# Kernel tuning notes

Measured on AMD Instinct MI355X. Metric: run time of the kernel, lower is better.

## Reference

```python
import jax, jax.numpy as jnp
import numpy as np

VOCAB = 21128; EMBED = 768; D_MODEL = 256; H = 100; NTAGS = 21; B = 32; T = 256


def setup_inputs() -> dict:
    key = jax.random.key(0)
    ks = jax.random.split(key, 18)
    n = lambda k, s, sc=0.05: jax.random.normal(k, s, dtype=jnp.float32) * sc
    return {
        "words": jax.random.randint(ks[0], (B, T), 0, VOCAB),
        "target": jax.random.randint(ks[1], (B, T), 0, NTAGS),
        "embed_table": n(ks[2], (VOCAB, EMBED), 1.0),
        "in_fc_w": n(ks[3], (D_MODEL, EMBED)),
        "in_fc_b": n(ks[4], (D_MODEL,)),
        "Wih0": n(ks[5], (2, 4 * H, D_MODEL)),
        "Whh0": n(ks[6], (2, 4 * H, H)),
        "bih0": n(ks[7], (2, 4 * H)),
        "bhh0": n(ks[8], (2, 4 * H)),
        "Wih1": n(ks[9], (2, 4 * H, 2 * H)),
        "Whh1": n(ks[10], (2, 4 * H, H)),
        "bih1": n(ks[11], (2, 4 * H)),
        "bhh1": n(ks[12], (2, 4 * H)),
        "out_w": n(ks[13], (NTAGS, 2 * H)),
        "out_b": n(ks[14], (NTAGS,)),
        "trans": n(ks[15], (NTAGS, NTAGS)),
        "start_s": n(ks[16], (NTAGS,)),
        "end_s": n(ks[17], (NTAGS,)),
    }


def _lstm_dir(x, Wih, Whh, bih, bhh, reverse):
    # x: (T, B, D); torch LSTM gate order i, f, g, o
    Bsz, Hd = x.shape[1], Whh.shape[1]
    pre = jnp.einsum('tbd,gd->tbg', x, Wih) + bih  # precompute input projection

    def step(carry, p):
        h, c = carry
        g = p + h @ Whh.T + bhh
        i, f, gg, o = jnp.split(g, 4, axis=-1)
        c = jax.nn.sigmoid(f) * c + jax.nn.sigmoid(i) * jnp.tanh(gg)
        h = jax.nn.sigmoid(o) * jnp.tanh(c)
        return (h, c), h

    init = (jnp.zeros((Bsz, Hd), x.dtype), jnp.zeros((Bsz, Hd), x.dtype))
    _, hs = jax.lax.scan(step, init, pre, reverse=reverse)
    return hs


def _bilstm(x, layers):
    h = x
    for (Wih, Whh, bih, bhh) in layers:  # fixed small loop over num_layers
        f = _lstm_dir(h, Wih[0], Whh[0], bih[0], bhh[0], False)
        b = _lstm_dir(h, Wih[1], Whh[1], bih[1], bhh[1], True)
        h = jnp.concatenate([f, b], axis=-1)
    return h


def _crf_loss(logits, tags, mask, trans, start_s, end_s):
    # fastNLP ConditionalRandomField loss: normalizer - gold_score, per batch elem
    lt = jnp.swapaxes(logits, 0, 1)          # (T, B, N)
    tt = tags.T                               # (T, B)
    mt = mask.T.astype(logits.dtype)          # (T, B)
    alpha0 = lt[0] + start_s

    def step(alpha, inp):
        emit, m = inp
        tmp = alpha[:, :, None] + trans[None] + emit[:, None, :]  # (B, N, N)
        new = jax.nn.logsumexp(tmp, axis=1)
        return jnp.where(m[:, None] > 0, new, alpha), None

    alpha, _ = jax.lax.scan(step, alpha0, (lt[1:], mt[1:]))
    normalizer = jax.nn.logsumexp(alpha + end_s, axis=1)  # (B,)

    emit_sc = jnp.take_along_axis(lt, tt[..., None], axis=2)[..., 0] * mt
    trans_sc = trans[tt[:-1], tt[1:]] * mt[1:]
    seq_lens = mask.sum(axis=1)
    last_idx = jnp.maximum(seq_lens - 1, 0)
    last_tags = tags[jnp.arange(tags.shape[0]), last_idx]
    gold = emit_sc.sum(0) + trans_sc.sum(0) + start_s[tt[0]] + end_s[last_tags]
    return normalizer - gold


def reference(words, target, embed_table, in_fc_w, in_fc_b, Wih0, Whh0, bih0, bhh0,
              Wih1, Whh1, bih1, bhh1, out_w, out_b, trans, start_s, end_s):
    mask = words != 0
    x = embed_table[words]                       # (B, T, E)
    x = x @ in_fc_w.T + in_fc_b                  # (B, T, D)
    x = jnp.swapaxes(x, 0, 1)                    # (T, B, D)
    h = _bilstm(x, [(Wih0, Whh0, bih0, bhh0), (Wih1, Whh1, bih1, bhh1)])
    h = jnp.swapaxes(h, 0, 1)                    # (B, T, 2H); dropout is identity at eval
    logits = jax.nn.log_softmax(h @ out_w.T + out_b, axis=-1)
    return _crf_loss(logits, target, mask, trans, start_s, end_s)  # (B,)
```

## Files before the change

### kernel.cpp

```cpp
#include <hip/hip_runtime.h>
#include <hip/hip_bf16.h>

#define VOCAB 21128
#define EMBED 768
#define DMODEL 256
#define HID 100
#define NTAGS 21
#define BB 32
#define TT 256
#define NTOK (BB*TT)

typedef float f32x4 __attribute__((ext_vector_type(4)));
typedef unsigned int u32x4 __attribute__((ext_vector_type(4)));
typedef short s16x8 __attribute__((ext_vector_type(8)));

__device__ __forceinline__ float sigm(float x) { return 1.0f / (1.0f + __expf(-x)); }
__device__ __forceinline__ float tanh_(float x) { return 2.0f / (1.0f + __expf(-2.0f * x)) - 1.0f; }

__device__ __forceinline__ unsigned int bfr(float x) {
    unsigned int u = __float_as_uint(x);
    return (u + 0x7fffu + ((u >> 16) & 1u)) >> 16;
}
__device__ __forceinline__ unsigned int bfpack(float lo, float hi) {
    return (bfr(hi) << 16) | bfr(lo);
}
__device__ __forceinline__ unsigned int cvtpk(float lo, float hi) {
    unsigned int r;
    asm("v_cvt_pk_bf16_f32 %0, %1, %2" : "=v"(r) : "v"(lo), "v"(hi));
    return r;
}
__device__ __forceinline__ s16x8 asfrag(u32x4 v) {
    union { u32x4 u; s16x8 s; } x; x.u = v; return x.s;
}

#define BAR() do { \
    asm volatile("s_waitcnt lgkmcnt(0)" ::: "memory"); \
    __builtin_amdgcn_s_barrier(); \
    __builtin_amdgcn_sched_barrier(0); \
} while (0)

__global__ __launch_bounds__(256) void gemm_mfma(
    const float* __restrict__ A, int lda,
    const float* __restrict__ B, int ldb,
    const float* __restrict__ bias1, const float* __restrict__ bias2,
    float* __restrict__ C, int ldc,
    int N, int K,
    const int* __restrict__ gatherWords, int permGates)
{
    __shared__ unsigned int As_[2][4096];
    __shared__ unsigned int Bs_[2][2048];

    const int tid = threadIdx.x;
    const int row0 = blockIdx.x * 128;
    const int col0 = blockIdx.y * 64;
    const int lane = tid & 63;
    const int wave = tid >> 6;
    const int wr = wave >> 1, wc = wave & 1;
    const int nsteps = (K + 63) >> 6;

    const float* arow[8]; int aoff[8]; int kqA[8];
    #pragma unroll
    for (int j = 0; j < 8; ++j) {
        int v = tid + 256 * j;
        int row = v >> 4, kq = v & 15;
        int grow = row0 + row;
        const float* ap;
        if (gatherWords) {
            int widx = gatherWords[(grow & 31) * TT + (grow >> 5)];
            ap = A + (size_t)widx * lda;
        } else {
            ap = A + (size_t)grow * lda;
        }
        arow[j] = ap + 4 * kq;
        aoff[j] = (row >> 4) * 512 + (kq >> 3) * 256 + ((kq >> 1) & 3) * 64
                + (row & 15) * 4 + (kq & 1) * 2;
        kqA[j] = kq;
    }
    const float* brow[4]; int boff[4]; int bok[4]; int kqB[4];
    #pragma unroll
    for (int j = 0; j < 4; ++j) {
        int v = tid + 256 * j;
        int r = v >> 4, kq = v & 15;
        int gcol = col0 + r;
        bok[j] = (gcol < N);
        int src = bok[j] ? gcol : 0;
        if (permGates && bok[j]) {
            int d2 = (gcol >= 400) ? 1 : 0;
            int rr = gcol - d2 * 400;
            src = d2 * 400 + (rr & 3) * 100 + (rr >> 2);
        }
        brow[j] = B + (size_t)src * ldb + 4 * kq;
        boff[j] = (r >> 4) * 512 + (kq >> 3) * 256 + ((kq >> 1) & 3) * 64
                + (r & 15) * 4 + (kq & 1) * 2;
        kqB[j] = kq;
    }

    {
        #pragma unroll
        for (int j = 0; j < 8; ++j) {
            f32x4 v = {0.f,0.f,0.f,0.f};
            if (4 * kqA[j] < K) v = *(const f32x4*)(arow[j]);
            As_[0][aoff[j]]     = cvtpk(v.x, v.y);
            As_[0][aoff[j] + 1] = cvtpk(v.z, v.w);
        }
        #pragma unroll
        for (int j = 0; j < 4; ++j) {
            f32x4 v = {0.f,0.f,0.f,0.f};
            if (bok[j] && 4 * kqB[j] < K) v = *(const f32x4*)(brow[j]);
            Bs_[0][boff[j]]     = cvtpk(v.x, v.y);
            Bs_[0][boff[j] + 1] = cvtpk(v.z, v.w);
        }
    }
    BAR();

    f32x4 acc[4][2] = {};

    for (int s = 0; s < nsteps; ++s) {
        const int cur = s & 1, nxt = cur ^ 1;

        f32x4 la[8], lb[4];
        if (s + 1 < nsteps) {
            const int kb = (s + 1) * 64;
            #pragma unroll
            for (int j = 0; j < 8; ++j) {
                la[j] = (f32x4){0.f,0.f,0.f,0.f};
                if (kb + 4 * kqA[j] < K) la[j] = *(const f32x4*)(arow[j] + kb);
            }
            #pragma unroll
            for (int j = 0; j < 4; ++j) {
                lb[j] = (f32x4){0.f,0.f,0.f,0.f};
                if (bok[j] && kb + 4 * kqB[j] < K) lb[j] = *(const f32x4*)(brow[j] + kb);
            }
        }

        u32x4 af[2][4], bf2[2][2];
        #pragma unroll
        for (int f = 0; f < 2; ++f) {
            #pragma unroll
            for (int mt = 0; mt < 4; ++mt)
                af[f][mt] = *(const u32x4*)&As_[cur][(4 * wr + mt) * 512 + f * 256 + lane * 4];
            #pragma unroll
            for (int nt = 0; nt < 2; ++nt)
                bf2[f][nt] = *(const u32x4*)&Bs_[cur][(2 * wc + nt) * 512 + f * 256 + lane * 4];
        }
        #pragma unroll
        for (int f = 0; f < 2; ++f)
            #pragma unroll
            for (int mt = 0; mt < 4; ++mt)
                #pragma unroll
                for (int nt = 0; nt < 2; ++nt)
                    acc[mt][nt] = __builtin_amdgcn_mfma_f32_16x16x32_bf16(
                        asfrag(af[f][mt]), asfrag(bf2[f][nt]), acc[mt][nt], 0, 0, 0);

        if (s + 1 < nsteps) {
            #pragma unroll
            for (int j = 0; j < 8; ++j) {
                As_[nxt][aoff[j]]     = cvtpk(la[j].x, la[j].y);
                As_[nxt][aoff[j] + 1] = cvtpk(la[j].z, la[j].w);
            }
            #pragma unroll
            for (int j = 0; j < 4; ++j) {
                Bs_[nxt][boff[j]]     = cvtpk(lb[j].x, lb[j].y);
                Bs_[nxt][boff[j] + 1] = cvtpk(lb[j].z, lb[j].w);
            }
        }
        BAR();
    }

    const int r4 = (lane >> 4) * 4;
    const int cl = lane & 15;
    #pragma unroll
    for (int nt = 0; nt < 2; ++nt) {
        int gcol = col0 + (2 * wc + nt) * 16 + cl;
        if (gcol < N) {
            int src = gcol;
            if (permGates) {
                int d2 = (gcol >= 400) ? 1 : 0;
                int rr = gcol - d2 * 400;
                src = d2 * 400 + (rr & 3) * 100 + (rr >> 2);
            }
            float bv = bias1[src];
            if (bias2) bv += bias2[src];
            #pragma unroll
            for (int mt = 0; mt < 4; ++mt) {
                int grow = row0 + (4 * wr + mt) * 16 + r4;
                #pragma unroll
                for (int r = 0; r < 4; ++r)
                    C[(size_t)(grow + r) * ldc + gcol] = acc[mt][nt][r] + bv;
            }
        }
    }
}

#define STASH_FRAG(SS, F, A0,A1,A2,A3) { \
    int tile = base + (SS); if (tile > 24) tile = 24; \
    int row16 = 16*tile + m16; \
    const float* srcp = Whh + (size_t)(dir*400 + (row16 & 3)*100 + (row16 >> 2)) * HID; \
    const int k0 = 32*(F) + 8*g4; \
    f32x4 fa = {0.f,0.f,0.f,0.f}, fb = {0.f,0.f,0.f,0.f}; \
    if (k0 < HID) fa = *(const f32x4*)(srcp + k0); \
    if (k0 + 4 < HID) fb = *(const f32x4*)(srcp + k0 + 4); \
    unsigned p0 = bfpack(fa.x, fa.y), p1 = bfpack(fa.z, fa.w); \
    unsigned p2 = bfpack(fb.x, fb.y), p3 = bfpack(fb.z, fb.w); \
    asm volatile("v_accvgpr_write_b32 a" #A0 ", %0\n\t" \
                 "v_accvgpr_write_b32 a" #A1 ", %1\n\t" \
                 "v_accvgpr_write_b32 a" #A2 ", %2\n\t" \
                 "v_accvgpr_write_b32 a" #A3 ", %3" \
                 :: "v"(p0), "v"(p1), "v"(p2), "v"(p3) \
                 : "a" #A0, "a" #A1, "a" #A2, "a" #A3); }

#define MF(ACC, BF, A0, A3) \
    asm volatile("v_mfma_f32_16x16x32_bf16 %0, a[" #A0 ":" #A3 "], %1, %0" \
                 : "+v"(ACC) : "v"(BF));

#define LOADCHUNK(K2) { \
    const int s0_ = 16 * (K2); \
    _Pragma("unroll") \
    for (int j = 0; j < 7; ++j) { \
        if (okj[j]) { \
            int tg = dir ? (TT - 1 - (s0_ + sicj[j])) : (s0_ + sicj[j]); \
            rr[j] = *(const f32x4*)(pre + (size_t)(tg * BB + b) * 800 + dir * 400 + 4 * gqj[j]); \
        } \
    } }

#define WRITECHUNK(BUF) { \
    _Pragma("unroll") \
    for (int j = 0; j < 7; ++j) { \
        if (okj[j]) { \
            float* p_ = &preS[(BUF) * 6400 + sicj[j] * 400 + gqj[j]]; \
            p_[0]   = rr[j].x; \
            p_[100] = rr[j].y; \
            p_[200] = rr[j].z; \
            p_[300] = rr[j].w; \
        } \
    } }

#define LSTM_STEP(SIC) { \
    const int t_ = dir ? (TT - 1 - (s0 + (SIC))) : (s0 + (SIC)); \
    const int i_ = t_ * BB + b; \
    const u32x4* hb_ = (const u32x4*)&h16[(SIC) & 1][0]; \
    u32x4 bf0 = hb_[g4], bf1 = hb_[4+g4], bf2 = hb_[8+g4], bf3 = hb_[12+g4]; \
    const float* pp_ = &preS[curbase + (SIC) * 400 + my_u]; \
    float px = pp_[0], py = pp_[100], pz = pp_[200], pw = pp_[300]; \
    f32x4 acc0 = {0.f,0.f,0.f,0.f}, acc1 = {0.f,0.f,0.f,0.f}; \
    f32x4 acc2 = {0.f,0.f,0.f,0.f}, acc3 = {0.f,0.f,0.f,0.f}; \
    f32x4 acc4 = {0.f,0.f,0.f,0.f}, acc5 = {0.f,0.f,0.f,0.f}; \
    f32x4 acc6 = {0.f,0.f,0.f,0.f}; \
    asm volatile("s_nop 1"); \
    MF(acc0, bf0, 0, 3)    MF(acc1, bf0, 16, 19)  MF(acc2, bf0, 32, 35) \
    MF(acc3, bf0, 48, 51)  MF(acc4, bf0, 64, 67)  MF(acc5, bf0, 80, 83) \
    MF(acc6, bf0, 96, 99) \
    MF(acc0, bf1, 4, 7)    MF(acc1, bf1, 20, 23)  MF(acc2, bf1, 36, 39) \
    MF(acc3, bf1, 52, 55)  MF(acc4, bf1, 68, 71)  MF(acc5, bf1, 84, 87) \
    MF(acc6, bf1, 100, 103) \
    MF(acc0, bf2, 8, 11)   MF(acc1, bf2, 24, 27)  MF(acc2, bf2, 40, 43) \
    MF(acc3, bf2, 56, 59)  MF(acc4, bf2, 72, 75)  MF(acc5, bf2, 88, 91) \
    MF(acc6, bf2, 104, 107) \
    MF(acc0, bf3, 12, 15)  MF(acc1, bf3, 28, 31)  MF(acc2, bf3, 44, 47) \
    MF(acc3, bf3, 60, 63)  MF(acc4, bf3, 76, 79)  MF(acc5, bf3, 92, 95) \
    MF(acc6, bf3, 108, 111) \
    asm volatile("s_nop 7\n\ts_nop 7"); \
    f32x4 t01 = (slot_sel & 1) ? acc1 : acc0; \
    f32x4 t23 = (slot_sel & 1) ? acc3 : acc2; \
    f32x4 t45 = (slot_sel & 1) ? acc5 : acc4; \
    f32x4 u0 = (slot_sel & 2) ? t23 : t01; \
    f32x4 u1 = (slot_sel & 2) ? acc6 : t45; \
    f32x4 sel = (slot_sel & 4) ? u1 : u0; \
    float igt = sigm(sel.x + px); \
    float fgt = sigm(sel.y + py); \
    float ggt = tanh_(sel.z + pz); \
    float ogt = sigm(sel.w + pw); \
    c = fgt * c + igt * ggt; \
    float h = ogt * tanh_(c); \
    if (writer) { \
        h16[((SIC) + 1) & 1][my_u] = (unsigned short)bfr(h); \
        hout[(size_t)i_ * 200 + dir * HID + my_u] = h; \
    } \
    BAR(); }

__global__ __launch_bounds__(256, 1) void lstm_mfma(
    const float* __restrict__ pre,
    const float* __restrict__ Whh,
    float* __restrict__ hout)
{
    const int dir = blockIdx.x >> 5;
    const int b = blockIdx.x & 31;
    const int tid = threadIdx.x;
    const int wave = tid >> 6;
    const int lane = tid & 63;
    const int m16 = lane & 15;
    const int g4 = lane >> 4;
    const int slot_sel = lane & 7;

    const int base = (wave == 0) ? 0 : (wave == 1) ? 7 : (wave == 2) ? 13 : 19;

    __shared__ alignas(16) unsigned short h16[2][128];
    __shared__ alignas(16) float preS[2 * 6400];

    STASH_FRAG(0,0, 0,1,2,3)      STASH_FRAG(0,1, 4,5,6,7)
    STASH_FRAG(0,2, 8,9,10,11)    STASH_FRAG(0,3, 12,13,14,15)
    STASH_FRAG(1,0, 16,17,18,19)  STASH_FRAG(1,1, 20,21,22,23)
    STASH_FRAG(1,2, 24,25,26,27)  STASH_FRAG(1,3, 28,29,30,31)
    STASH_FRAG(2,0, 32,33,34,35)  STASH_FRAG(2,1, 36,37,38,39)
    STASH_FRAG(2,2, 40,41,42,43)  STASH_FRAG(2,3, 44,45,46,47)
    STASH_FRAG(3,0, 48,49,50,51)  STASH_FRAG(3,1, 52,53,54,55)
    STASH_FRAG(3,2, 56,57,58,59)  STASH_FRAG(3,3, 60,61,62,63)
    STASH_FRAG(4,0, 64,65,66,67)  STASH_FRAG(4,1, 68,69,70,71)
    STASH_FRAG(4,2, 72,73,74,75)  STASH_FRAG(4,3, 76,77,78,79)
    STASH_FRAG(5,0, 80,81,82,83)  STASH_FRAG(5,1, 84,85,86,87)
    STASH_FRAG(5,2, 88,89,90,91)  STASH_FRAG(5,3, 92,93,94,95)
    STASH_FRAG(6,0, 96,97,98,99)  STASH_FRAG(6,1, 100,101,102,103)
    STASH_FRAG(6,2, 104,105,106,107) STASH_FRAG(6,3, 108,109,110,111)

    if (tid < 128) { h16[0][tid] = 0; h16[1][tid] = 0; }

    int my_tile = base + ((slot_sel < 7) ? slot_sel : 6);
    if (my_tile > 24) my_tile = 24;
    const int my_u = 4 * my_tile + g4;
    const int ow_lim = (wave == 0) ? 7 : 6;
    const bool writer = (slot_sel < ow_lim) && ((lane & 8) == 0);

    int sicj[7], gqj[7]; bool okj[7];
    #pragma unroll
    for (int j = 0; j < 7; ++j) {
        int idx = tid + 256 * j;
        okj[j] = (idx < 1600);
        int ic = okj[j] ? idx : 0;
        sicj[j] = ic / 100;
        gqj[j] = ic - 100 * sicj[j];
    }

    float c = 0.f;
    f32x4 rr[7];

    LOADCHUNK(0)
    WRITECHUNK(0)
    LOADCHUNK(1)
    BAR();

    for (int k = 0; k < 16; ++k) {
        const int s0 = 16 * k;
        const int curbase = (k & 1) * 6400;
        LSTM_STEP(0)  LSTM_STEP(1)  LSTM_STEP(2)  LSTM_STEP(3)
        LSTM_STEP(4)  LSTM_STEP(5)  LSTM_STEP(6)  LSTM_STEP(7)
        LSTM_STEP(8)  LSTM_STEP(9)  LSTM_STEP(10) LSTM_STEP(11)
        LSTM_STEP(12) LSTM_STEP(13) LSTM_STEP(14) LSTM_STEP(15)
        if (k < 15) { WRITECHUNK((k & 1) ^ 1) }
        if (k < 14) { LOADCHUNK(k + 2) }
        BAR();
    }
}

__global__ __launch_bounds__(256) void logits_lsm(
    const float* __restrict__ h1,
    const float* __restrict__ out_w,
    const float* __restrict__ out_b,
    float* __restrict__ logits)
{
    const int lane = threadIdx.x & 63;
    const int wid = (blockIdx.x * 256 + threadIdx.x) >> 6;
    const int half = lane >> 5;
    const int n = lane & 31;
    const int i = wid * 2 + half;
    if (i >= NTOK) return;

    float acc = -1e30f;
    if (n < NTAGS) {
        acc = out_b[n];
        const float4* hr = (const float4*)(h1 + (size_t)i * 200);
        const float4* wr = (const float4*)(out_w + (size_t)n * 200);
        #pragma unroll
        for (int e = 0; e < 50; ++e) {
            float4 h4 = hr[e], w4 = wr[e];
            acc += h4.x * w4.x + h4.y * w4.y + h4.z * w4.z + h4.w * w4.w;
        }
    }
    float m = acc;
    for (int off = 16; off > 0; off >>= 1) m = fmaxf(m, __shfl_xor(m, off, 32));
    float ex = (n < NTAGS) ? __expf(acc - m) : 0.f;
    float s = ex;
    for (int off = 16; off > 0; off >>= 1) s += __shfl_xor(s, off, 32);
    if (n < NTAGS) logits[(size_t)i * NTAGS + n] = acc - m - __logf(s);
}

__global__ __launch_bounds__(64) void crf_kernel(
    const float* __restrict__ logits,
    const int* __restrict__ words,
    const int* __restrict__ target,
    const float* __restrict__ trans,
    const float* __restrict__ start_s,
    const float* __restrict__ end_s,
    float* __restrict__ out)
{
    const int b = blockIdx.x;
    const int j = threadIdx.x;
    const int j21 = (j < NTAGS) ? j : (NTAGS - 1);

    float tcol[NTAGS];
    #pragma unroll
    for (int i = 0; i < NTAGS; ++i) tcol[i] = (j < NTAGS) ? trans[i * NTAGS + j] : 0.f;

    const int w0 = words[b * TT +   0 + j];
    const int w1 = words[b * TT +  64 + j];
    const int w2 = words[b * TT + 128 + j];
    const int w3 = words[b * TT + 192 + j];

    float alpha = (j < NTAGS) ? (logits[(size_t)(0 * BB + b) * NTAGS + j] + start_s[j]) : -1e30f;
    float e_cur = logits[(size_t)(1 * BB + b) * NTAGS + j21];

#define CRF_CHUNK(WREG, T0) \
    for (int u = ((T0) == 0 ? 1 : 0); u < 64; ++u) { \
        const int t = (T0) + u; \
        float e_nxt = 0.f; \
        if (t + 1 < TT) e_nxt = logits[(size_t)((t + 1) * BB + b) * NTAGS + j21]; \
        if (__shfl(WREG, u, 64) != 0) { \
            float v[NTAGS]; \
            _Pragma("unroll") \
            for (int i2 = 0; i2 < NTAGS; ++i2) \
                v[i2] = __shfl(alpha, i2, 64) + tcol[i2]; \
            float m0[11]; \
            _Pragma("unroll") \
            for (int p = 0; p < 10; ++p) m0[p] = fmaxf(v[2*p], v[2*p+1]); \
            m0[10] = v[20]; \
            float m1[6]; \
            _Pragma("unroll") \
            for (int p = 0; p < 5; ++p) m1[p] = fmaxf(m0[2*p], m0[2*p+1]); \
            m1[5] = m0[10]; \
            float m2a = fmaxf(m1[0], m1[1]), m2b = fmaxf(m1[2], m1[3]), m2c = fmaxf(m1[4], m1[5]); \
            float mx = fmaxf(fmaxf(m2a, m2b), m2c); \
            float e[NTAGS]; \
            _Pragma("unroll") \
            for (int i2 = 0; i2 < NTAGS; ++i2) e[i2] = __expf(v[i2] - mx); \
            float s0[11]; \
            _Pragma("unroll") \
            for (int p = 0; p < 10; ++p) s0[p] = e[2*p] + e[2*p+1]; \
            s0[10] = e[20]; \
            float s1[6]; \
            _Pragma("unroll") \
            for (int p = 0; p < 5; ++p) s1[p] = s0[2*p] + s0[2*p+1]; \
            s1[5] = s0[10]; \
            float ss = ((s1[0] + s1[1]) + (s1[2] + s1[3])) + (s1[4] + s1[5]); \
            float na = mx + __logf(ss) + e_cur; \
            alpha = (j < NTAGS) ? na : -1e30f; \
        } \
        e_cur = e_nxt; \
    }

    CRF_CHUNK(w0, 0)
    CRF_CHUNK(w1, 64)
    CRF_CHUNK(w2, 128)
    CRF_CHUNK(w3, 192)
#undef CRF_CHUNK

    float val = (j < NTAGS) ? (alpha + end_s[j]) : -1e30f;
    float mx = val;
    for (int off = 32; off > 0; off >>= 1) mx = fmaxf(mx, __shfl_xor(mx, off, 64));
    float s = (j < NTAGS) ? __expf(val - mx) : 0.f;
    for (int off = 32; off > 0; off >>= 1) s += __shfl_xor(s, off, 64);
    float norm = mx + __logf(s);

    float gold = 0.f, slen = 0.f;
    for (int t = j; t < TT; t += 64) {
        int tg = target[b * TT + t];
        bool m = (words[b * TT + t] != 0);
        if (m) {
            gold += logits[(size_t)(t * BB + b) * NTAGS + tg];
            slen += 1.f;
            if (t >= 1) gold += trans[target[b * TT + t - 1] * NTAGS + tg];
        }
    }
    for (int off = 32; off > 0; off >>= 1) {
        gold += __shfl_xor(gold, off, 64);
        slen += __shfl_xor(slen, off, 64);
    }
    if (j == 0) {
        int len = (int)slen;
        int last = (len > 0) ? (len - 1) : 0;
        int last_tag = target[b * TT + last];
        gold += start_s[target[b * TT + 0]] + end_s[last_tag];
        out[b] = norm - gold;
    }
}

extern "C" void kernel_launch(void* const* d_in, const int* in_sizes, int n_in,
                              void* d_out, int out_size, void* d_ws, size_t ws_size,
                              hipStream_t stream) {
    const int*   words   = (const int*)  d_in[0];
    const int*   target  = (const int*)  d_in[1];
    const float* embed   = (const float*)d_in[2];
    const float* in_fc_w = (const float*)d_in[3];
    const float* in_fc_b = (const float*)d_in[4];
    const float* Wih0    = (const float*)d_in[5];
    const float* Whh0    = (const float*)d_in[6];
    const float* bih0    = (const float*)d_in[7];
    const float* bhh0    = (const float*)d_in[8];
    const float* Wih1    = (const float*)d_in[9];
    const float* Whh1    = (const float*)d_in[10];
    const float* bih1    = (const float*)d_in[11];
    const float* bhh1    = (const float*)d_in[12];
    const float* out_w   = (const float*)d_in[13];
    const float* out_b   = (const float*)d_in[14];
    const float* trans   = (const float*)d_in[15];
    const float* start_s = (const float*)d_in[16];
    const float* end_s   = (const float*)d_in[17];
    float* out = (float*)d_out;

    float* ws = (float*)d_ws;
    float* x      = ws;
    float* pre    = ws + 2097152;
    float* h0     = ws + 8650752;
    float* h1     = ws;
    float* logits = ws + 1638400;

    gemm_mfma<<<dim3(64, 4), 256, 0, stream>>>(
        embed, EMBED, in_fc_w, EMBED, in_fc_b, nullptr,
        x, DMODEL, DMODEL, EMBED, words, 0);

    gemm_mfma<<<dim3(64, 13), 256, 0, stream>>>(
        x, DMODEL, Wih0, DMODEL, bih0, bhh0,
        pre, 800, 800, DMODEL, nullptr, 1);

    lstm_mfma<<<64, 256, 0, stream>>>(pre, Whh0, h0);

    gemm_mfma<<<dim3(64, 13), 256, 0, stream>>>(
        h0, 200, Wih1, 200, bih1, bhh1,
        pre, 800, 800, 200, nullptr, 1);

    lstm_mfma<<<64, 256, 0, stream>>>(pre, Whh1, h1);

    logits_lsm<<<NTOK / 8, 256, 0, stream>>>(h1, out_w, out_b, logits);

    crf_kernel<<<BB, 64, 0, stream>>>(logits, words, target, trans, start_s, end_s, out);
}
```

Baseline: 570.8 us.

## Batch 16 sequences per LSTM block using full MFMA N dimension

Restructures the recurrent LSTM kernel so each block handles 16 batch elements at once, putting them in the MFMA N dimension instead of running one sequence per block with the B operand mostly idle. The grid shrinks from 64 to 4 blocks. Every lane now runs the epilogue for all 7 accumulator tiles, and the LDS staging of precomputed gates is replaced by direct per-lane register prefetch two steps ahead. The trade is far fewer active CUs and more per-step epilogue work per lane, in exchange for no longer wasting MFMA throughput and no longer needing the LDS staging pass.

Result: slower. 1.339 ms (+134.6%).

```diff
diff --git a/kernel.cpp b/kernel.cpp
--- a/kernel.cpp
+++ b/kernel.cpp
@@ -193,7 +193,7 @@
 }
 
 #define STASH_FRAG(SS, F, A0,A1,A2,A3) { \
-    int tile = base + (SS); if (tile > 24) tile = 24; \
+    int tile = base + (SS); \
     int row16 = 16*tile + m16; \
     const float* srcp = Whh + (size_t)(dir*400 + (row16 & 3)*100 + (row16 >> 2)) * HID; \
     const int k0 = 32*(F) + 8*g4; \
@@ -213,68 +213,49 @@
     asm volatile("v_mfma_f32_16x16x32_bf16 %0, a[" #A0 ":" #A3 "], %1, %0" \
                  : "+v"(ACC) : "v"(BF));
 
-#define LOADCHUNK(K2) { \
-    const int s0_ = 16 * (K2); \
-    _Pragma("unroll") \
-    for (int j = 0; j < 7; ++j) { \
-        if (okj[j]) { \
-            int tg = dir ? (TT - 1 - (s0_ + sicj[j])) : (s0_ + sicj[j]); \
-            rr[j] = *(const f32x4*)(pre + (size_t)(tg * BB + b) * 800 + dir * 400 + 4 * gqj[j]); \
-        } \
-    } }
-
-#define WRITECHUNK(BUF) { \
-    _Pragma("unroll") \
-    for (int j = 0; j < 7; ++j) { \
-        if (okj[j]) { \
-            float* p_ = &preS[(BUF) * 6400 + sicj[j] * 400 + gqj[j]]; \
-            p_[0]   = rr[j].x; \
-            p_[100] = rr[j].y; \
-            p_[200] = rr[j].z; \
-            p_[300] = rr[j].w; \
-        } \
-    } }
-
-#define LSTM_STEP(SIC) { \
-    const int t_ = dir ? (TT - 1 - (s0 + (SIC))) : (s0 + (SIC)); \
-    const int i_ = t_ * BB + b; \
-    const u32x4* hb_ = (const u32x4*)&h16[(SIC) & 1][0]; \
-    u32x4 bf0 = hb_[g4], bf1 = hb_[4+g4], bf2 = hb_[8+g4], bf3 = hb_[12+g4]; \
-    const float* pp_ = &preS[curbase + (SIC) * 400 + my_u]; \
-    float px = pp_[0], py = pp_[100], pz = pp_[200], pw = pp_[300]; \
-    f32x4 acc0 = {0.f,0.f,0.f,0.f}, acc1 = {0.f,0.f,0.f,0.f}; \
-    f32x4 acc2 = {0.f,0.f,0.f,0.f}, acc3 = {0.f,0.f,0.f,0.f}; \
-    f32x4 acc4 = {0.f,0.f,0.f,0.f}, acc5 = {0.f,0.f,0.f,0.f}; \
-    f32x4 acc6 = {0.f,0.f,0.f,0.f}; \
+#define EPI(PP, SL) { \
+    f32x4 gg = ac##SL + PP##SL; \
+    float ii = sigm(gg.x); \
+    float ff = sigm(gg.y); \
+    float zz = tanh_(gg.z); \
+    float oo = sigm(gg.w); \
+    c##SL = ff * c##SL + ii * zz; \
+    float hh = oo * tanh_(c##SL); \
+    h16[nb_][bloc][u_base + 4*(SL)] = (unsigned short)bfr(hh); \
+    hout[(size_t)(t_ * BB + bb) * 200 + dir * HID + u_base + 4*(SL)] = hh; \
+}
+
+#define LSTEP(PP, S) { \
+    const int t_ = dir ? (TT - 1 - (S)) : (S); \
+    const int nb_ = ((S) + 1) & 1; \
+    const u32x4* hb_ = (const u32x4*)&h16[(S) & 1][bloc][0]; \
+    u32x4 bf0 = hb_[g4], bf1 = hb_[4 + g4], bf2 = hb_[8 + g4], bf3 = hb_[12 + g4]; \
+    f32x4 ac0 = {0.f,0.f,0.f,0.f}, ac1 = {0.f,0.f,0.f,0.f}; \
+    f32x4 ac2 = {0.f,0.f,0.f,0.f}, ac3 = {0.f,0.f,0.f,0.f}; \
+    f32x4 ac4 = {0.f,0.f,0.f,0.f}, ac5 = {0.f,0.f,0.f,0.f}; \
+    f32x4 ac6 = {0.f,0.f,0.f,0.f}; \
     asm volatile("s_nop 1"); \
-    MF(acc0, bf0, 0, 3)    MF(acc1, bf0, 16, 19)  MF(acc2, bf0, 32, 35) \
-    MF(acc3, bf0, 48, 51)  MF(acc4, bf0, 64, 67)  MF(acc5, bf0, 80, 83) \
-    MF(acc6, bf0, 96, 99) \
-    MF(acc0, bf1, 4, 7)    MF(acc1, bf1, 20, 23)  MF(acc2, bf1, 36, 39) \
-    MF(acc3, bf1, 52, 55)  MF(acc4, bf1, 68, 71)  MF(acc5, bf1, 84, 87) \
-    MF(acc6, bf1, 100, 103) \
-    MF(acc0, bf2, 8, 11)   MF(acc1, bf2, 24, 27)  MF(acc2, bf2, 40, 43) \
-    MF(acc3, bf2, 56, 59)  MF(acc4, bf2, 72, 75)  MF(acc5, bf2, 88, 91) \
-    MF(acc6, bf2, 104, 107) \
-    MF(acc0, bf3, 12, 15)  MF(acc1, bf3, 28, 31)  MF(acc2, bf3, 44, 47) \
-    MF(acc3, bf3, 60, 63)  MF(acc4, bf3, 76, 79)  MF(acc5, bf3, 92, 95) \
-    MF(acc6, bf3, 108, 111) \
+    MF(ac0, bf0, 0, 3)    MF(ac1, bf0, 16, 19)  MF(ac2, bf0, 32, 35) \
+    MF(ac3, bf0, 48, 51)  MF(ac4, bf0, 64, 67)  MF(ac5, bf0, 80, 83) \
+    MF(ac6, bf0, 96, 99) \
+    MF(ac0, bf1, 4, 7)    MF(ac1, bf1, 20, 23)  MF(ac2, bf1, 36, 39) \
+    MF(ac3, bf1, 52, 55)  MF(ac4, bf1, 68, 71)  MF(ac5, bf1, 84, 87) \
+    MF(ac6, bf1, 100, 103) \
+    MF(ac0, bf2, 8, 11)   MF(ac1, bf2, 24, 27)  MF(ac2, bf2, 40, 43) \
+    MF(ac3, bf2, 56, 59)  MF(ac4, bf2, 72, 75)  MF(ac5, bf2, 88, 91) \
+    MF(ac6, bf2, 104, 107) \
+    MF(ac0, bf3, 12, 15)  MF(ac1, bf3, 28, 31)  MF(ac2, bf3, 44, 47) \
+    MF(ac3, bf3, 60, 63)  MF(ac4, bf3, 76, 79)  MF(ac5, bf3, 92, 95) \
+    MF(ac6, bf3, 108, 111) \
     asm volatile("s_nop 7\n\ts_nop 7"); \
-    f32x4 t01 = (slot_sel & 1) ? acc1 : acc0; \
-    f32x4 t23 = (slot_sel & 1) ? acc3 : acc2; \
-    f32x4 t45 = (slot_sel & 1) ? acc5 : acc4; \
-    f32x4 u0 = (slot_sel & 2) ? t23 : t01; \
-    f32x4 u1 = (slot_sel & 2) ? acc6 : t45; \
-    f32x4 sel = (slot_sel & 4) ? u1 : u0; \
-    float igt = sigm(sel.x + px); \
-    float fgt = sigm(sel.y + py); \
-    float ggt = tanh_(sel.z + pz); \
-    float ogt = sigm(sel.w + pw); \
-    c = fgt * c + igt * ggt; \
-    float h = ogt * tanh_(c); \
-    if (writer) { \
-        h16[((SIC) + 1) & 1][my_u] = (unsigned short)bfr(h); \
-        hout[(size_t)i_ * 200 + dir * HID + my_u] = h; \
+    EPI(PP, 0) EPI(PP, 1) EPI(PP, 2) EPI(PP, 3) EPI(PP, 4) EPI(PP, 5) EPI(PP, 6) \
+    if ((S) + 2 < TT) { \
+        const int tn_ = dir ? (TT - 3 - (S)) : ((S) + 2); \
+        const float* pq_ = pre_lane + (size_t)tn_ * 25600; \
+        PP##0 = *(const f32x4*)(pq_);      PP##1 = *(const f32x4*)(pq_ + 16); \
+        PP##2 = *(const f32x4*)(pq_ + 32); PP##3 = *(const f32x4*)(pq_ + 48); \
+        PP##4 = *(const f32x4*)(pq_ + 64); PP##5 = *(const f32x4*)(pq_ + 80); \
+        PP##6 = *(const f32x4*)(pq_ + 96); \
     } \
     BAR(); }
 
@@ -283,19 +264,19 @@
     const float* __restrict__ Whh,
     float* __restrict__ hout)
 {
-    const int dir = blockIdx.x >> 5;
-    const int b = blockIdx.x & 31;
+    const int dir = blockIdx.x >> 1;
+    const int bg = blockIdx.x & 1;
     const int tid = threadIdx.x;
     const int wave = tid >> 6;
     const int lane = tid & 63;
     const int m16 = lane & 15;
     const int g4 = lane >> 4;
-    const int slot_sel = lane & 7;
-
-    const int base = (wave == 0) ? 0 : (wave == 1) ? 7 : (wave == 2) ? 13 : 19;
-
-    __shared__ alignas(16) unsigned short h16[2][128];
-    __shared__ alignas(16) float preS[2 * 6400];
+    const int bloc = lane & 15;
+    const int bb = bg * 16 + bloc;
+
+    const int base = (wave == 0) ? 0 : (wave == 1) ? 7 : (wave == 2) ? 13 : 18;
+
+    __shared__ alignas(16) unsigned short h16[2][16][136];
 
     STASH_FRAG(0,0, 0,1,2,3)      STASH_FRAG(0,1, 4,5,6,7)
     STASH_FRAG(0,2, 8,9,10,11)    STASH_FRAG(0,3, 12,13,14,15)
@@ -312,42 +293,36 @@
     STASH_FRAG(6,0, 96,97,98,99)  STASH_FRAG(6,1, 100,101,102,103)
     STASH_FRAG(6,2, 104,105,106,107) STASH_FRAG(6,3, 108,109,110,111)
 
-    if (tid < 128) { h16[0][tid] = 0; h16[1][tid] = 0; }
-
-    int my_tile = base + ((slot_sel < 7) ? slot_sel : 6);
-    if (my_tile > 24) my_tile = 24;
-    const int my_u = 4 * my_tile + g4;
-    const int ow_lim = (wave == 0) ? 7 : 6;
-    const bool writer = (slot_sel < ow_lim) && ((lane & 8) == 0);
-
-    int sicj[7], gqj[7]; bool okj[7];
-    #pragma unroll
-    for (int j = 0; j < 7; ++j) {
-        int idx = tid + 256 * j;
-        okj[j] = (idx < 1600);
-        int ic = okj[j] ? idx : 0;
-        sicj[j] = ic / 100;
-        gqj[j] = ic - 100 * sicj[j];
-    }
-
-    float c = 0.f;
-    f32x4 rr[7];
-
-    LOADCHUNK(0)
-    WRITECHUNK(0)
-    LOADCHUNK(1)
+    for (int i = tid; i < 2 * 16 * 136; i += 256)
+        ((unsigned short*)h16)[i] = 0;
+
+    const int u_base = 4 * base + g4;
+
+    const float* pre_lane = pre + (size_t)bb * 800 + dir * 400 + 16 * base + 4 * g4;
+
+    float c0 = 0.f, c1 = 0.f, c2 = 0.f, c3 = 0.f, c4 = 0.f, c5 = 0.f, c6 = 0.f;
+
+    f32x4 pa0, pa1, pa2, pa3, pa4, pa5, pa6;
+    f32x4 pb0, pb1, pb2, pb3, pb4, pb5, pb6;
+    {
+        const int t0 = dir ? (TT - 1) : 0;
+        const float* pq = pre_lane + (size_t)t0 * 25600;
+        pa0 = *(const f32x4*)(pq);      pa1 = *(const f32x4*)(pq + 16);
+        pa2 = *(const f32x4*)(pq + 32); pa3 = *(const f32x4*)(pq + 48);
+        pa4 = *(const f32x4*)(pq + 64); pa5 = *(const f32x4*)(pq + 80);
+        pa6 = *(const f32x4*)(pq + 96);
+        const int t1 = dir ? (TT - 2) : 1;
+        const float* pq2 = pre_lane + (size_t)t1 * 25600;
+        pb0 = *(const f32x4*)(pq2);      pb1 = *(const f32x4*)(pq2 + 16);
+        pb2 = *(const f32x4*)(pq2 + 32); pb3 = *(const f32x4*)(pq2 + 48);
+        pb4 = *(const f32x4*)(pq2 + 64); pb5 = *(const f32x4*)(pq2 + 80);
+        pb6 = *(const f32x4*)(pq2 + 96);
+    }
     BAR();
 
-    for (int k = 0; k < 16; ++k) {
-        const int s0 = 16 * k;
-        const int curbase = (k & 1) * 6400;
-        LSTM_STEP(0)  LSTM_STEP(1)  LSTM_STEP(2)  LSTM_STEP(3)
-        LSTM_STEP(4)  LSTM_STEP(5)  LSTM_STEP(6)  LSTM_STEP(7)
-        LSTM_STEP(8)  LSTM_STEP(9)  LSTM_STEP(10) LSTM_STEP(11)
-        LSTM_STEP(12) LSTM_STEP(13) LSTM_STEP(14) LSTM_STEP(15)
-        if (k < 15) { WRITECHUNK((k & 1) ^ 1) }
-        if (k < 14) { LOADCHUNK(k + 2) }
-        BAR();
+    for (int s = 0; s < TT; s += 2) {
+        LSTEP(pa, s)
+        LSTEP(pb, s + 1)
     }
 }
 
@@ -520,13 +495,13 @@
         x, DMODEL, Wih0, DMODEL, bih0, bhh0,
         pre, 800, 800, DMODEL, nullptr, 1);
 
-    lstm_mfma<<<64, 256, 0, stream>>>(pre, Whh0, h0);
+    lstm_mfma<<<4, 256, 0, stream>>>(pre, Whh0, h0);
 
     gemm_mfma<<<dim3(64, 13), 256, 0, stream>>>(
         h0, 200, Wih1, 200, bih1, bhh1,
         pre, 800, 800, 200, nullptr, 1);
 
-    lstm_mfma<<<64, 256, 0, stream>>>(pre, Whh1, h1);
+    lstm_mfma<<<4, 256, 0, stream>>>(pre, Whh1, h1);
 
     logits_lsm<<<NTOK / 8, 256, 0, stream>>>(h1, out_w, out_b, logits);
 
```
